# Kernel tuning notes

Hardware: AMD Instinct MI355X
Metric: run time of the kernel (lower is better)

Reference implementation:

```python
import jax, jax.numpy as jnp
import numpy as np

N = 1024
H = 128


def setup_inputs() -> dict:
    key = jax.random.key(0)
    ks = jax.random.split(key, 12)
    s = 0.05
    inp = {
        "h": jax.random.normal(ks[0], (N, H), dtype=jnp.float32),
        "x": jax.random.normal(ks[1], (N, 2), dtype=jnp.float32),
        "batch": jnp.zeros((N,), dtype=jnp.int32),
        # attention projections (torch Linear: y = x @ W.T + b)
        "Wq": jax.random.normal(ks[2], (H, H), dtype=jnp.float32) * s,
        "bq": jnp.zeros((H,), dtype=jnp.float32),
        "Wk": jax.random.normal(ks[3], (H, H), dtype=jnp.float32) * s,
        "bk": jnp.zeros((H,), dtype=jnp.float32),
        "Wv": jax.random.normal(ks[4], (H, H), dtype=jnp.float32) * s,
        "bv": jnp.zeros((H,), dtype=jnp.float32),
        # edge_mlp: Linear(2,H) -> ReLU -> Linear(H,H)
        "We1": jax.random.normal(ks[5], (H, 2), dtype=jnp.float32) * s,
        "be1": jnp.zeros((H,), dtype=jnp.float32),
        "We2": jax.random.normal(ks[6], (H, H), dtype=jnp.float32) * s,
        "be2": jnp.zeros((H,), dtype=jnp.float32),
        # coord_mlp: Linear(H,1)
        "Wc": jax.random.normal(ks[7], (1, H), dtype=jnp.float32) * s,
        "bc": jnp.zeros((1,), dtype=jnp.float32),
    }
    return inp


def reference(h, x, batch, Wq, bq, Wk, bk, Wv, bv, We1, be1, We2, be2, Wc, bc):
    # rel_x[i, j] = x[i] - x[j]  -> [N, N, 2]
    rel_x = x[:, None, :] - x[None, :, :]
    # edge MLP over all pairs -> [N, N, H]
    edge_feat = jax.nn.relu(rel_x @ We1.T + be1) @ We2.T + be2
    q = h @ Wq.T + bq  # [N, H]
    k = h @ Wk.T + bk
    v = h @ Wv.T + bv
    scale = 1.0 / np.sqrt(float(H)).astype(np.float32)
    attn = jax.nn.softmax((q @ k.T) * scale, axis=-1)  # [N, N]
    agg_h = attn @ v  # [N, H]
    coord_w = edge_feat @ Wc.T + bc  # [N, N, 1]
    # weighted coordinate diffusion, summed over neighbors j (axis=1)
    delta_x = jnp.sum(attn[:, :, None] * (coord_w * rel_x), axis=1)  # [N, 2]
    return (h + agg_h, x + delta_x)
```

## Files before the change

### kernel.cpp

```cpp
#include <hip/hip_runtime.h>
#include <hip/hip_fp16.h>

#define NN 1024
#define HH 128
#define QR 2
#define TPB 512
#define RPB 2

typedef _Float16 f16x2_t __attribute__((ext_vector_type(2)));

__device__ __forceinline__ float dot2(__half2 a, __half2 b, float c) {
#if __has_builtin(__builtin_amdgcn_fdot2)
  return __builtin_amdgcn_fdot2(__builtin_bit_cast(f16x2_t, a),
                                __builtin_bit_cast(f16x2_t, b), c, false);
#else
  return fmaf(__low2float(a), __low2float(b),
              fmaf(__high2float(a), __high2float(b), c));
#endif
}

__device__ __forceinline__ __half2 relu2(__half2 a) {
#if __has_builtin(__builtin_elementwise_max)
  f16x2_t v = __builtin_bit_cast(f16x2_t, a);
  f16x2_t z = {(_Float16)0.f, (_Float16)0.f};
  return __builtin_bit_cast(__half2, __builtin_elementwise_max(v, z));
#else
  unsigned int av = __builtin_bit_cast(unsigned int, a);
  unsigned int rv;
  asm("v_pk_max_f16 %0, %1, 0" : "=v"(rv) : "v"(av));
  return __builtin_bit_cast(__half2, rv);
#endif
}

__device__ __forceinline__ float2 wmax2(float2 v) {
#pragma unroll
  for (int off = 1; off < 64; off <<= 1) {
    v.x = fmaxf(v.x, __shfl_xor(v.x, off));
    v.y = fmaxf(v.y, __shfl_xor(v.y, off));
  }
  return v;
}
__device__ __forceinline__ float2 wsum2(float2 v) {
#pragma unroll
  for (int off = 1; off < 64; off <<= 1) {
    v.x += __shfl_xor(v.x, off);
    v.y += __shfl_xor(v.y, off);
  }
  return v;
}

__global__ __launch_bounds__(128)
void prep_kernel(const float* __restrict__ Wq, const float* __restrict__ Wk,
                 const float* __restrict__ Wv, const float* __restrict__ We1,
                 const float* __restrict__ be1, const float* __restrict__ We2,
                 const float* __restrict__ be2, const float* __restrict__ Wc,
                 const float* __restrict__ bc,
                 float* __restrict__ WqT, float* __restrict__ WkT,
                 float* __restrict__ WvT, float* __restrict__ epack,
                 float* __restrict__ c0,
                 __half2* __restrict__ aB, __half2* __restrict__ bB,
                 __half2* __restrict__ uB) {
  __shared__ float su[HH];
  const int d = blockIdx.x;
  const int o = threadIdx.x;
  WqT[d * HH + o] = Wq[o * HH + d];
  WkT[d * HH + o] = Wk[o * HH + d];
  WvT[d * HH + o] = Wv[o * HH + d];
  if (d == 0) {
    float uu = 0.f;
    for (int e = 0; e < HH; ++e) uu = fmaf(Wc[e], We2[e * HH + o], uu);
    su[o] = uu;
    epack[o * 4 + 0] = We1[2 * o];
    epack[o * 4 + 1] = We1[2 * o + 1];
    epack[o * 4 + 2] = be1[o];
    epack[o * 4 + 3] = uu;
    if (o == 0) {
      float s = bc[0];
      for (int e = 0; e < HH; ++e) s = fmaf(Wc[e], be2[e], s);
      c0[0] = s;
    }
    __syncthreads();
    if (o < 64) {
      aB[o] = __halves2half2(__float2half(We1[4 * o]), __float2half(We1[4 * o + 2]));
      bB[o] = __halves2half2(__float2half(We1[4 * o + 1]), __float2half(We1[4 * o + 3]));
      uB[o] = __halves2half2(__float2half(su[2 * o]), __float2half(su[2 * o + 1]));
    }
  }
}

__global__ __launch_bounds__(128)
void qkv_kernel(const float* __restrict__ hin,
                const float* __restrict__ WqT, const float* __restrict__ WkT,
                const float* __restrict__ WvT,
                const float* __restrict__ bq, const float* __restrict__ bk,
                const float* __restrict__ bv,
                __half* __restrict__ q16, __half* __restrict__ k8,
                float* __restrict__ vF) {
  __shared__ __align__(16) float hT[HH][QR];
  const int tid = threadIdx.x;
  const int i0 = blockIdx.x * QR;
#pragma unroll
  for (int r = 0; r < QR; ++r) hT[tid][r] = hin[(i0 + r) * HH + tid];
  __syncthreads();
  float qa0 = 0.f, qa1 = 0.f, ka0 = 0.f, ka1 = 0.f, va0 = 0.f, va1 = 0.f;
#pragma unroll 4
  for (int d = 0; d < HH; ++d) {
    float wq = WqT[d * HH + tid];
    float wk = WkT[d * HH + tid];
    float wv = WvT[d * HH + tid];
    float2 hh = *(const float2*)&hT[d][0];
    qa0 = fmaf(hh.x, wq, qa0); qa1 = fmaf(hh.y, wq, qa1);
    ka0 = fmaf(hh.x, wk, ka0); ka1 = fmaf(hh.y, wk, ka1);
    va0 = fmaf(hh.x, wv, va0); va1 = fmaf(hh.y, wv, va1);
  }
  const float scale = 0.08838834764831845f;
  float bqv = bq[tid], bkv = bk[tid], bvv = bv[tid];
  q16[(i0 + 0) * HH + tid] = __float2half((qa0 + bqv) * scale);
  q16[(i0 + 1) * HH + tid] = __float2half((qa1 + bqv) * scale);
  const int c = tid >> 3, slot = tid & 7;
  k8[(size_t)((c * NN + i0 + 0) << 3) + slot] = __float2half(ka0 + bkv);
  k8[(size_t)((c * NN + i0 + 1) << 3) + slot] = __float2half(ka1 + bkv);
  vF[(i0 + 0) * HH + tid] = va0 + bvv;
  vF[(i0 + 1) * HH + tid] = va1 + bvv;
}

__global__ __launch_bounds__(TPB, 4)
void fused_kernel(const __half* __restrict__ q16, const __half* __restrict__ k8,
                  const float* __restrict__ vF, const float* __restrict__ hin,
                  const float* __restrict__ x, const float* __restrict__ epack,
                  const __half2* __restrict__ aB, const __half2* __restrict__ bB,
                  const __half2* __restrict__ uB, const float* __restrict__ c0p,
                  float* __restrict__ out_h, float* __restrict__ out_x) {
  __shared__ __align__(16) float2 sp2[NN];
  __shared__ __align__(16) float4 sredh[16][32][2];
  __shared__ __half2 stab[RPB][64];
  __shared__ float2 sredm[8], sreds[8], sredx[8], sredy[8];

  const int tid = threadIdx.x;
  const int lane = tid & 63;
  const int wid = tid >> 6;
  const int i0 = blockIdx.x * RPB;
  const int j0 = tid, j1 = tid + TPB;

  if (tid < 2 * 64) {
    const int r = tid & 1, tp = tid >> 1;
    const float4 ea = ((const float4*)epack)[2 * tp];
    const float4 eb = ((const float4*)epack)[2 * tp + 1];
    float xrx = x[(i0 + r) * 2 + 0], xry = x[(i0 + r) * 2 + 1];
    stab[r][tp] = __halves2half2(
        __float2half(fmaf(ea.x, xrx, fmaf(ea.y, xry, ea.z))),
        __float2half(fmaf(eb.x, xrx, fmaf(eb.y, xry, eb.z))));
  }

  const __half2* q0p = (const __half2*)(q16 + (size_t)(i0 + 0) * HH);
  const __half2* q1p = (const __half2*)(q16 + (size_t)(i0 + 1) * HH);
  const float4* k84 = (const float4*)k8;
  float s00 = 0.f, s01 = 0.f, s10 = 0.f, s11 = 0.f;
#pragma unroll
  for (int c = 0; c < 16; ++c) {
    float4 ka = k84[c * NN + j0];
    float4 kb = k84[c * NN + j1];
    __half2 a0 = __builtin_bit_cast(__half2, ka.x);
    __half2 a1 = __builtin_bit_cast(__half2, ka.y);
    __half2 a2 = __builtin_bit_cast(__half2, ka.z);
    __half2 a3 = __builtin_bit_cast(__half2, ka.w);
    __half2 b0 = __builtin_bit_cast(__half2, kb.x);
    __half2 b1 = __builtin_bit_cast(__half2, kb.y);
    __half2 b2 = __builtin_bit_cast(__half2, kb.z);
    __half2 b3 = __builtin_bit_cast(__half2, kb.w);
    __half2 qa0 = q0p[4 * c + 0], qa1 = q0p[4 * c + 1];
    __half2 qa2 = q0p[4 * c + 2], qa3 = q0p[4 * c + 3];
    __half2 qb0 = q1p[4 * c + 0], qb1 = q1p[4 * c + 1];
    __half2 qb2 = q1p[4 * c + 2], qb3 = q1p[4 * c + 3];
    s00 = dot2(a0, qa0, s00); s00 = dot2(a1, qa1, s00);
    s00 = dot2(a2, qa2, s00); s00 = dot2(a3, qa3, s00);
    s01 = dot2(b0, qa0, s01); s01 = dot2(b1, qa1, s01);
    s01 = dot2(b2, qa2, s01); s01 = dot2(b3, qa3, s01);
    s10 = dot2(a0, qb0, s10); s10 = dot2(a1, qb1, s10);
    s10 = dot2(a2, qb2, s10); s10 = dot2(a3, qb3, s10);
    s11 = dot2(b0, qb0, s11); s11 = dot2(b1, qb1, s11);
    s11 = dot2(b2, qb2, s11); s11 = dot2(b3, qb3, s11);
  }

  float2 mv = wmax2(make_float2(fmaxf(s00, s01), fmaxf(s10, s11)));
  if (lane == 0) sredm[wid] = mv;
  __syncthreads();
  float2 mm = sredm[0];
#pragma unroll
  for (int w2 = 1; w2 < 8; ++w2) {
    float2 t2 = sredm[w2];
    mm.x = fmaxf(mm.x, t2.x); mm.y = fmaxf(mm.y, t2.y);
  }

  float e00 = __expf(s00 - mm.x), e01 = __expf(s01 - mm.x);
  float e10 = __expf(s10 - mm.y), e11 = __expf(s11 - mm.y);
  sp2[j0] = make_float2(e00, e10);
  sp2[j1] = make_float2(e01, e11);
  float2 sv = wsum2(make_float2(e00 + e01, e10 + e11));
  if (lane == 0) sreds[wid] = sv;
  __syncthreads();
  float2 ssv = sreds[0];
#pragma unroll
  for (int w2 = 1; w2 < 8; ++w2) { ssv.x += sreds[w2].x; ssv.y += sreds[w2].y; }
  const float inv0 = 1.f / ssv.x, inv1 = 1.f / ssv.y;

  {
    const int op2 = tid & 31;
    const int cc = tid >> 5;
    float4 ar0 = make_float4(0.f, 0.f, 0.f, 0.f);
    float4 ar1 = make_float4(0.f, 0.f, 0.f, 0.f);
#pragma unroll 4
    for (int jj = 0; jj < NN / 16; ++jj) {
      int jv = cc * (NN / 16) + jj;
      float4 vv = ((const float4*)vF)[jv * 32 + op2];
      float2 pp = sp2[jv];
      ar0.x = fmaf(pp.x, vv.x, ar0.x); ar0.y = fmaf(pp.x, vv.y, ar0.y);
      ar0.z = fmaf(pp.x, vv.z, ar0.z); ar0.w = fmaf(pp.x, vv.w, ar0.w);
      ar1.x = fmaf(pp.y, vv.x, ar1.x); ar1.y = fmaf(pp.y, vv.y, ar1.y);
      ar1.z = fmaf(pp.y, vv.z, ar1.z); ar1.w = fmaf(pp.y, vv.w, ar1.w);
    }
    sredh[cc][op2][0] = ar0;
    sredh[cc][op2][1] = ar1;
  }

  float2 xja = *(const float2*)&x[2 * j0];
  float2 xjb = *(const float2*)&x[2 * j1];
  __half2 xax = __float2half2_rn(xja.x), xay = __float2half2_rn(xja.y);
  __half2 xbx = __float2half2_rn(xjb.x), xby = __float2half2_rn(xjb.y);
  float wa00 = 0.f, wa01 = 0.f, wa10 = 0.f, wa11 = 0.f;
#pragma unroll 8
  for (int tp = 0; tp < 64; ++tp) {
    __half2 a2 = aB[tp], b2 = bB[tp], u2 = uB[tp];
    __half2 wA = __hfma2(a2, xax, __hmul2(b2, xay));
    __half2 wB = __hfma2(a2, xbx, __hmul2(b2, xby));
    __half2 s0t = stab[0][tp], s1t = stab[1][tp];
    wa00 = dot2(u2, relu2(__hsub2(s0t, wA)), wa00);
    wa01 = dot2(u2, relu2(__hsub2(s0t, wB)), wa01);
    wa10 = dot2(u2, relu2(__hsub2(s1t, wA)), wa10);
    wa11 = dot2(u2, relu2(__hsub2(s1t, wB)), wa11);
  }
  const float c0v = c0p[0];
  float cw00 = e00 * (wa00 + c0v), cw01 = e01 * (wa01 + c0v);
  float cw10 = e10 * (wa10 + c0v), cw11 = e11 * (wa11 + c0v);
  float xi0x = x[i0 * 2 + 0], xi0y = x[i0 * 2 + 1];
  float xi1x = x[i0 * 2 + 2], xi1y = x[i0 * 2 + 3];
  float2 rx = wsum2(make_float2(
      fmaf(cw00, xi0x - xja.x, cw01 * (xi0x - xjb.x)),
      fmaf(cw10, xi1x - xja.x, cw11 * (xi1x - xjb.x))));
  float2 ry = wsum2(make_float2(
      fmaf(cw00, xi0y - xja.y, cw01 * (xi0y - xjb.y)),
      fmaf(cw10, xi1y - xja.y, cw11 * (xi1y - xjb.y))));
  if (lane == 0) { sredx[wid] = rx; sredy[wid] = ry; }

  __syncthreads();

  if (tid < 2 * HH) {
    const int f = tid & 127, r = tid >> 7;
    const int o2 = f >> 2, fi = f & 3;
    float acc = 0.f;
#pragma unroll
    for (int c2 = 0; c2 < 16; ++c2)
      acc += ((const float*)&sredh[c2][o2][r])[fi];
    float invr = r ? inv1 : inv0;
    out_h[(i0 + r) * HH + f] = hin[(i0 + r) * HH + f] + acc * invr;
  }
  if (tid < 2) {
    const int r = tid;
    float sx = 0.f, sy = 0.f;
#pragma unroll
    for (int w2 = 0; w2 < 8; ++w2) {
      sx += r ? sredx[w2].y : sredx[w2].x;
      sy += r ? sredy[w2].y : sredy[w2].x;
    }
    float invr = r ? inv1 : inv0;
    out_x[(i0 + r) * 2 + 0] = x[(i0 + r) * 2 + 0] + sx * invr;
    out_x[(i0 + r) * 2 + 1] = x[(i0 + r) * 2 + 1] + sy * invr;
  }
}

extern "C" void kernel_launch(void* const* d_in, const int* in_sizes, int n_in,
                              void* d_out, int out_size, void* d_ws, size_t ws_size,
                              hipStream_t stream) {
  (void)in_sizes; (void)n_in; (void)out_size; (void)ws_size;
  const float* h   = (const float*)d_in[0];
  const float* x   = (const float*)d_in[1];
  const float* Wq  = (const float*)d_in[3];
  const float* bq  = (const float*)d_in[4];
  const float* Wk  = (const float*)d_in[5];
  const float* bk  = (const float*)d_in[6];
  const float* Wv  = (const float*)d_in[7];
  const float* bv  = (const float*)d_in[8];
  const float* We1 = (const float*)d_in[9];
  const float* be1 = (const float*)d_in[10];
  const float* We2 = (const float*)d_in[11];
  const float* be2 = (const float*)d_in[12];
  const float* Wc  = (const float*)d_in[13];
  const float* bc  = (const float*)d_in[14];

  float* ws   = (float*)d_ws;
  float* WqT  = ws;
  float* WkT  = WqT + HH * HH;
  float* WvT  = WkT + HH * HH;
  float* ep   = WvT + HH * HH;
  float* c0   = ep + 4 * HH;
  __half* q16 = (__half*)(c0 + 8);
  __half* k8  = q16 + NN * HH;
  float* vF   = (float*)(k8 + NN * HH);
  __half2* aB = (__half2*)(vF + NN * HH);
  __half2* bB = aB + 64;
  __half2* uB = bB + 64;

  float* out_h = (float*)d_out;
  float* out_x = out_h + NN * HH;

  prep_kernel<<<dim3(HH), dim3(128), 0, stream>>>(
      Wq, Wk, Wv, We1, be1, We2, be2, Wc, bc, WqT, WkT, WvT, ep, c0, aB, bB, uB);
  qkv_kernel<<<dim3(NN / QR), dim3(128), 0, stream>>>(
      h, WqT, WkT, WvT, bq, bk, bv, q16, k8, vF);
  fused_kernel<<<dim3(NN / RPB), dim3(TPB), 0, stream>>>(
      q16, k8, vF, h, x, ep, aB, bB, uB, c0, out_h, out_x);
}
```

Measured before the change: 124.4 us.

## Store V in fp16 and reorder fused kernel to overlap edge MLP with softmax

```diff
diff --git a/kernel.cpp b/kernel.cpp
--- a/kernel.cpp
+++ b/kernel.cpp
@@ -95,7 +95,7 @@
                 const float* __restrict__ bq, const float* __restrict__ bk,
                 const float* __restrict__ bv,
                 __half* __restrict__ q16, __half* __restrict__ k8,
-                float* __restrict__ vF) {
+                __half* __restrict__ v16) {
   __shared__ __align__(16) float hT[HH][QR];
   const int tid = threadIdx.x;
   const int i0 = blockIdx.x * QR;
@@ -120,20 +120,20 @@
   const int c = tid >> 3, slot = tid & 7;
   k8[(size_t)((c * NN + i0 + 0) << 3) + slot] = __float2half(ka0 + bkv);
   k8[(size_t)((c * NN + i0 + 1) << 3) + slot] = __float2half(ka1 + bkv);
-  vF[(i0 + 0) * HH + tid] = va0 + bvv;
-  vF[(i0 + 1) * HH + tid] = va1 + bvv;
+  v16[(i0 + 0) * HH + tid] = __float2half(va0 + bvv);
+  v16[(i0 + 1) * HH + tid] = __float2half(va1 + bvv);
 }
 
 __global__ __launch_bounds__(TPB, 4)
 void fused_kernel(const __half* __restrict__ q16, const __half* __restrict__ k8,
-                  const float* __restrict__ vF, const float* __restrict__ hin,
+                  const __half* __restrict__ v16, const float* __restrict__ hin,
                   const float* __restrict__ x, const float* __restrict__ epack,
                   const __half2* __restrict__ aB, const __half2* __restrict__ bB,
                   const __half2* __restrict__ uB, const float* __restrict__ c0p,
                   float* __restrict__ out_h, float* __restrict__ out_x) {
   __shared__ __align__(16) float2 sp2[NN];
   __shared__ __align__(16) float4 sredh[16][32][2];
-  __shared__ __half2 stab[RPB][64];
+  __shared__ __align__(16) float2 stab2[64];
   __shared__ float2 sredm[8], sreds[8], sredx[8], sredy[8];
 
   const int tid = threadIdx.x;
@@ -142,15 +142,22 @@
   const int i0 = blockIdx.x * RPB;
   const int j0 = tid, j1 = tid + TPB;
 
-  if (tid < 2 * 64) {
-    const int r = tid & 1, tp = tid >> 1;
+  if (tid < 64) {
+    const int tp = tid;
     const float4 ea = ((const float4*)epack)[2 * tp];
     const float4 eb = ((const float4*)epack)[2 * tp + 1];
-    float xrx = x[(i0 + r) * 2 + 0], xry = x[(i0 + r) * 2 + 1];
-    stab[r][tp] = __halves2half2(
-        __float2half(fmaf(ea.x, xrx, fmaf(ea.y, xry, ea.z))),
-        __float2half(fmaf(eb.x, xrx, fmaf(eb.y, xry, eb.z))));
-  }
+    float x0x = x[i0 * 2 + 0], x0y = x[i0 * 2 + 1];
+    float x1x = x[i0 * 2 + 2], x1y = x[i0 * 2 + 3];
+    __half2 hA = __halves2half2(
+        __float2half(fmaf(ea.x, x0x, fmaf(ea.y, x0y, ea.z))),
+        __float2half(fmaf(eb.x, x0x, fmaf(eb.y, x0y, eb.z))));
+    __half2 hB = __halves2half2(
+        __float2half(fmaf(ea.x, x1x, fmaf(ea.y, x1y, ea.z))),
+        __float2half(fmaf(eb.x, x1x, fmaf(eb.y, x1y, eb.z))));
+    stab2[tp] = make_float2(__builtin_bit_cast(float, hA),
+                            __builtin_bit_cast(float, hB));
+  }
+  __syncthreads();
 
   const __half2* q0p = (const __half2*)(q16 + (size_t)(i0 + 0) * HH);
   const __half2* q1p = (const __half2*)(q16 + (size_t)(i0 + 1) * HH);
@@ -182,47 +189,6 @@
     s11 = dot2(b2, qb2, s11); s11 = dot2(b3, qb3, s11);
   }
 
-  float2 mv = wmax2(make_float2(fmaxf(s00, s01), fmaxf(s10, s11)));
-  if (lane == 0) sredm[wid] = mv;
-  __syncthreads();
-  float2 mm = sredm[0];
-#pragma unroll
-  for (int w2 = 1; w2 < 8; ++w2) {
-    float2 t2 = sredm[w2];
-    mm.x = fmaxf(mm.x, t2.x); mm.y = fmaxf(mm.y, t2.y);
-  }
-
-  float e00 = __expf(s00 - mm.x), e01 = __expf(s01 - mm.x);
-  float e10 = __expf(s10 - mm.y), e11 = __expf(s11 - mm.y);
-  sp2[j0] = make_float2(e00, e10);
-  sp2[j1] = make_float2(e01, e11);
-  float2 sv = wsum2(make_float2(e00 + e01, e10 + e11));
-  if (lane == 0) sreds[wid] = sv;
-  __syncthreads();
-  float2 ssv = sreds[0];
-#pragma unroll
-  for (int w2 = 1; w2 < 8; ++w2) { ssv.x += sreds[w2].x; ssv.y += sreds[w2].y; }
-  const float inv0 = 1.f / ssv.x, inv1 = 1.f / ssv.y;
-
-  {
-    const int op2 = tid & 31;
-    const int cc = tid >> 5;
-    float4 ar0 = make_float4(0.f, 0.f, 0.f, 0.f);
-    float4 ar1 = make_float4(0.f, 0.f, 0.f, 0.f);
-#pragma unroll 4
-    for (int jj = 0; jj < NN / 16; ++jj) {
-      int jv = cc * (NN / 16) + jj;
-      float4 vv = ((const float4*)vF)[jv * 32 + op2];
-      float2 pp = sp2[jv];
-      ar0.x = fmaf(pp.x, vv.x, ar0.x); ar0.y = fmaf(pp.x, vv.y, ar0.y);
-      ar0.z = fmaf(pp.x, vv.z, ar0.z); ar0.w = fmaf(pp.x, vv.w, ar0.w);
-      ar1.x = fmaf(pp.y, vv.x, ar1.x); ar1.y = fmaf(pp.y, vv.y, ar1.y);
-      ar1.z = fmaf(pp.y, vv.z, ar1.z); ar1.w = fmaf(pp.y, vv.w, ar1.w);
-    }
-    sredh[cc][op2][0] = ar0;
-    sredh[cc][op2][1] = ar1;
-  }
-
   float2 xja = *(const float2*)&x[2 * j0];
   float2 xjb = *(const float2*)&x[2 * j1];
   __half2 xax = __float2half2_rn(xja.x), xay = __float2half2_rn(xja.y);
@@ -231,14 +197,34 @@
 #pragma unroll 8
   for (int tp = 0; tp < 64; ++tp) {
     __half2 a2 = aB[tp], b2 = bB[tp], u2 = uB[tp];
+    float2 st = stab2[tp];
+    __half2 s0t = __builtin_bit_cast(__half2, st.x);
+    __half2 s1t = __builtin_bit_cast(__half2, st.y);
     __half2 wA = __hfma2(a2, xax, __hmul2(b2, xay));
     __half2 wB = __hfma2(a2, xbx, __hmul2(b2, xby));
-    __half2 s0t = stab[0][tp], s1t = stab[1][tp];
     wa00 = dot2(u2, relu2(__hsub2(s0t, wA)), wa00);
     wa01 = dot2(u2, relu2(__hsub2(s0t, wB)), wa01);
     wa10 = dot2(u2, relu2(__hsub2(s1t, wA)), wa10);
     wa11 = dot2(u2, relu2(__hsub2(s1t, wB)), wa11);
   }
+
+  float2 mv = wmax2(make_float2(fmaxf(s00, s01), fmaxf(s10, s11)));
+  if (lane == 0) sredm[wid] = mv;
+  __syncthreads();
+  float2 mm = sredm[0];
+#pragma unroll
+  for (int w2 = 1; w2 < 8; ++w2) {
+    float2 t2 = sredm[w2];
+    mm.x = fmaxf(mm.x, t2.x); mm.y = fmaxf(mm.y, t2.y);
+  }
+
+  float e00 = __expf(s00 - mm.x), e01 = __expf(s01 - mm.x);
+  float e10 = __expf(s10 - mm.y), e11 = __expf(s11 - mm.y);
+  sp2[j0] = make_float2(e00, e10);
+  sp2[j1] = make_float2(e01, e11);
+  float2 sv = wsum2(make_float2(e00 + e01, e10 + e11));
+  if (lane == 0) sreds[wid] = sv;
+
   const float c0v = c0p[0];
   float cw00 = e00 * (wa00 + c0v), cw01 = e01 * (wa01 + c0v);
   float cw10 = e10 * (wa10 + c0v), cw11 = e11 * (wa11 + c0v);
@@ -251,7 +237,35 @@
       fmaf(cw00, xi0y - xja.y, cw01 * (xi0y - xjb.y)),
       fmaf(cw10, xi1y - xja.y, cw11 * (xi1y - xjb.y))));
   if (lane == 0) { sredx[wid] = rx; sredy[wid] = ry; }
-
+  __syncthreads();
+
+  float2 ssv = sreds[0];
+#pragma unroll
+  for (int w2 = 1; w2 < 8; ++w2) { ssv.x += sreds[w2].x; ssv.y += sreds[w2].y; }
+  const float inv0 = 1.f / ssv.x, inv1 = 1.f / ssv.y;
+
+  {
+    const int op2 = tid & 31;
+    const int cc = tid >> 5;
+    float4 ar0 = make_float4(0.f, 0.f, 0.f, 0.f);
+    float4 ar1 = make_float4(0.f, 0.f, 0.f, 0.f);
+#pragma unroll 4
+    for (int jj = 0; jj < NN / 16; ++jj) {
+      int jv = cc * (NN / 16) + jj;
+      float2 raw = ((const float2*)v16)[jv * 32 + op2];
+      __half2 v01 = __builtin_bit_cast(__half2, raw.x);
+      __half2 v23 = __builtin_bit_cast(__half2, raw.y);
+      float vx = __low2float(v01), vy = __high2float(v01);
+      float vz = __low2float(v23), vw = __high2float(v23);
+      float2 pp = sp2[jv];
+      ar0.x = fmaf(pp.x, vx, ar0.x); ar0.y = fmaf(pp.x, vy, ar0.y);
+      ar0.z = fmaf(pp.x, vz, ar0.z); ar0.w = fmaf(pp.x, vw, ar0.w);
+      ar1.x = fmaf(pp.y, vx, ar1.x); ar1.y = fmaf(pp.y, vy, ar1.y);
+      ar1.z = fmaf(pp.y, vz, ar1.z); ar1.w = fmaf(pp.y, vw, ar1.w);
+    }
+    sredh[cc][op2][0] = ar0;
+    sredh[cc][op2][1] = ar1;
+  }
   __syncthreads();
 
   if (tid < 2 * HH) {
@@ -305,8 +319,8 @@
   float* c0   = ep + 4 * HH;
   __half* q16 = (__half*)(c0 + 8);
   __half* k8  = q16 + NN * HH;
-  float* vF   = (float*)(k8 + NN * HH);
-  __half2* aB = (__half2*)(vF + NN * HH);
+  __half* v16 = k8 + NN * HH;
+  __half2* aB = (__half2*)(v16 + NN * HH);
   __half2* bB = aB + 64;
   __half2* uB = bB + 64;
 
@@ -316,7 +330,7 @@
   prep_kernel<<<dim3(HH), dim3(128), 0, stream>>>(
       Wq, Wk, Wv, We1, be1, We2, be2, Wc, bc, WqT, WkT, WvT, ep, c0, aB, bB, uB);
   qkv_kernel<<<dim3(NN / QR), dim3(128), 0, stream>>>(
-      h, WqT, WkT, WvT, bq, bk, bv, q16, k8, vF);
+      h, WqT, WkT, WvT, bq, bk, bv, q16, k8, v16);
   fused_kernel<<<dim3(NN / RPB), dim3(TPB), 0, stream>>>(
-      q16, k8, vF, h, x, ep, aB, bB, uB, c0, out_h, out_x);
-}
+      q16, k8, v16, h, x, ep, aB, bB, uB, c0, out_h, out_x);
+}
```

Result: slower. 131.6 us (+5.9%).
